# Kernel optimization log

Measured on AMD Instinct MI355X. Metric: run time of the kernel, lower is better.

Reference implementation:

```python
import jax, jax.numpy as jnp
import numpy as np
from jax import lax

N_NOTES, N_WORDS, BATCH = 64, 256, 32
WORDS_DIM, VOCAB = 128, 50000
OC, FW = 256, 3          # conv output channels, filter width
H, NCLS = 256, 2         # GRU hidden, target classes


def setup_inputs() -> dict:
    key = jax.random.key(0)
    ks = jax.random.split(key, 18)
    s = 0.05
    nrm = lambda k, shp: (jax.random.normal(k, shp, dtype=jnp.float32) * s)
    return {
        "mini_batch": jax.random.randint(ks[0], (N_NOTES, N_WORDS, BATCH), 0, VOCAB),
        "hidden_state": jnp.zeros((2, BATCH, H), jnp.float32),
        "embed_table": nrm(ks[1], (VOCAB, WORDS_DIM)),
        "conv_w": nrm(ks[2], (OC, 1, FW, WORDS_DIM)),
        "conv_b": nrm(ks[3], (OC,)),
        "w_ih_f": nrm(ks[4], (3 * H, OC)), "w_hh_f": nrm(ks[5], (3 * H, H)),
        "b_ih_f": nrm(ks[6], (3 * H,)),   "b_hh_f": nrm(ks[7], (3 * H,)),
        "w_ih_b": nrm(ks[8], (3 * H, OC)), "w_hh_b": nrm(ks[9], (3 * H, H)),
        "b_ih_b": nrm(ks[10], (3 * H,)),  "b_hh_b": nrm(ks[11], (3 * H,)),
        "W_note": nrm(ks[12], (2 * H, 2 * H)),
        "bias_note": nrm(ks[13], (2 * H,)),
        "proj_note": nrm(ks[14], (2 * H,)),
        "lin_w": nrm(ks[15], (NCLS, 2 * H)),
        "lin_b": nrm(ks[16], (NCLS,)),
    }


def _gru_scan(xs, h0, w_ih, w_hh, b_ih, b_hh, reverse=False):
    # xs: [N, B, in], h0: [B, H]; standard PyTorch GRU cell math.
    def step(h, x):
        gi = x @ w_ih.T + b_ih
        gh = h @ w_hh.T + b_hh
        ir, iz, i_n = jnp.split(gi, 3, axis=-1)
        hr, hz, h_n = jnp.split(gh, 3, axis=-1)
        r = jax.nn.sigmoid(ir + hr)
        z = jax.nn.sigmoid(iz + hz)
        n = jnp.tanh(i_n + r * h_n)
        h_new = (1.0 - z) * n + z * h
        return h_new, h_new
    _, ys = lax.scan(step, h0, xs, reverse=reverse)
    return ys  # [N, B, H]


def reference(mini_batch, hidden_state, embed_table, conv_w, conv_b,
              w_ih_f, w_hh_f, b_ih_f, b_hh_f,
              w_ih_b, w_hh_b, b_ih_b, b_hh_b,
              W_note, bias_note, proj_note, lin_w, lin_b):
    N, Wd, B = mini_batch.shape
    toks = mini_batch.transpose(0, 2, 1)                 # [N, B, Wd]
    emb = embed_table[toks]                              # [N, B, Wd, D] -- big gather
    x = emb.reshape(N * B, 1, Wd, WORDS_DIM)             # NCHW
    y = lax.conv_general_dilated(
        x, conv_w, window_strides=(1, 1),
        padding=((FW - 1, FW - 1), (0, 0)),
        dimension_numbers=("NCHW", "OIHW", "NCHW"))     # [N*B, OC, L, 1]
    y = jnp.tanh(y + conv_b[None, :, None, None])[..., 0]  # [N*B, OC, L]
    feat = y.max(axis=2).reshape(N, B, -1)               # max-pool over words -> [N, B, OC]

    out_f = _gru_scan(feat, hidden_state[0], w_ih_f, w_hh_f, b_ih_f, b_hh_f)
    out_b = _gru_scan(feat, hidden_state[1], w_ih_b, w_hh_b, b_ih_b, b_hh_b, reverse=True)
    out_note = jnp.concatenate([out_f, out_b], axis=-1)  # [N, B, 2H]

    # additive attention over notes (fused version of the per-step python loops)
    squish = jnp.tanh(jnp.einsum("nbd,de->nbe", out_note, W_note) + bias_note)
    attn = jnp.einsum("nbe,e->nb", squish, proj_note)    # [N, B]
    note_attn_norm = jax.nn.softmax(attn.T, axis=1)      # [B, N], softmax over notes
    note_attn_vectors = jnp.einsum("nb,nbd->bd", note_attn_norm.T, out_note)  # [B, 2H]
    final_map = note_attn_vectors @ lin_w.T + lin_b      # [B, NCLS]
    return (out_note, note_attn_norm, note_attn_vectors, final_map)
```

## Files before the change

kernel.cpp:

```cpp
#include <hip/hip_runtime.h>

#define NN 64
#define NW 256
#define NB 32
#define WD 128
#define OCH 256
#define HD 256
#define G3 768

typedef __attribute__((ext_vector_type(8))) __bf16 bf16x8;
typedef __attribute__((ext_vector_type(4))) __bf16 bf16x4;
typedef __attribute__((ext_vector_type(4))) float  f32x4;

__device__ __forceinline__ float sigm(float x){ return 1.f/(1.f + __expf(-x)); }
__device__ __forceinline__ float tanh_(float x){
  float xx = fminf(fmaxf(x, -15.f), 15.f);
  float e = __expf(-2.f*xx);
  return (1.f - e)/(1.f + e);
}
__device__ __forceinline__ bf16x8 pack8(f32x4 a, f32x4 b){
  bf16x8 v;
  v[0]=(__bf16)a[0]; v[1]=(__bf16)a[1]; v[2]=(__bf16)a[2]; v[3]=(__bf16)a[3];
  v[4]=(__bf16)b[0]; v[5]=(__bf16)b[1]; v[6]=(__bf16)b[2]; v[7]=(__bf16)b[3];
  return v;
}
__device__ __forceinline__ void gload_lds16(const void* g, void* l){
  __builtin_amdgcn_global_load_lds(
      (const __attribute__((address_space(1))) unsigned int*)g,
      (__attribute__((address_space(3))) unsigned int*)l, 16, 0, 0);
}

#define EMB_ELEMS 6400000
#define CW_ELEMS  98304
__global__ void k0_cvt(const float* __restrict__ emb, const float* __restrict__ cw,
                       __bf16* __restrict__ embb, __bf16* __restrict__ cwb)
{
  long e8 = ((long)blockIdx.x*256 + threadIdx.x)*8;
  if (e8 < EMB_ELEMS) {
    f32x4 a = *(const f32x4*)(emb + e8); f32x4 b = *(const f32x4*)(emb + e8 + 4);
    *(bf16x8*)(embb + e8) = pack8(a, b);
  } else if (e8 < EMB_ELEMS + CW_ELEMS) {
    long o = e8 - EMB_ELEMS;
    f32x4 a = *(const f32x4*)(cw + o); f32x4 b = *(const f32x4*)(cw + o + 4);
    *(bf16x8*)(cwb + o) = pack8(a, b);
  }
}

__global__ __launch_bounds__(512, 2) void k1_conv(
    const int* __restrict__ mb, const __bf16* __restrict__ embb,
    const __bf16* __restrict__ cwb, const float* __restrict__ cb,
    __bf16* __restrict__ feat)
{
  __shared__ int tok[NW];
  __shared__ __bf16 A[274*128];
  const int blk = blockIdx.x, n = blk >> 5, b = blk & 31;
  const int t = threadIdx.x, wv = t >> 6, l = t & 63;
  const int lo = l & 15, hi = l >> 4;
  if (t < NW) tok[t] = mb[(n*NW + t)*NB + b];
  if (t < 288) {
    int rr = t >> 4, c = t & 15;
    int row = (rr < 2) ? rr : (256 + rr);
    f32x4 z = {0.f,0.f,0.f,0.f};
    *(f32x4*)((char*)A + row*256 + c*16) = z;
  }
  __syncthreads();
  #pragma unroll
  for (int rr = 0; rr < 8; ++rr) {
    const int w = wv*32 + rr*4 + hi;
    const int row = w + 2;
    const __bf16* src = embb + (long)tok[w]*WD + ((lo ^ (row & 7)) << 3);
    gload_lds16(src, &A[(wv*32 + rr*4 + 2)*128]);
  }
  __syncthreads();
  const int ocb = wv*32;
  bf16x8 B[2][12];
  #pragma unroll
  for (int nt = 0; nt < 2; ++nt) {
    int oc = ocb + nt*16 + lo;
    #pragma unroll
    for (int kf = 0; kf < 12; ++kf)
      B[nt][kf] = *(const bf16x8*)(cwb + oc*384 + kf*32 + hi*8);
  }
  f32x4 mx0 = {-3e38f,-3e38f,-3e38f,-3e38f}, mx1 = mx0;
  for (int mt = 0; mt < 17; ++mt) {
    bf16x8 Af[12];
    const int lrow = mt*16 + lo;
    #pragma unroll
    for (int kf = 0; kf < 12; ++kf) {
      int prow = lrow + (kf >> 2);
      int ch = (kf & 3)*4 + hi;
      Af[kf] = *(const bf16x8*)((char*)A + prow*256 + ((ch ^ (prow & 7)) << 4));
    }
    f32x4 a0 = {0,0,0,0}, a1 = {0,0,0,0};
    #pragma unroll
    for (int kf = 0; kf < 12; ++kf) {
      a0 = __builtin_amdgcn_mfma_f32_16x16x32_bf16(Af[kf], B[0][kf], a0, 0,0,0);
      a1 = __builtin_amdgcn_mfma_f32_16x16x32_bf16(Af[kf], B[1][kf], a1, 0,0,0);
    }
    const int rbase = mt*16 + hi*4;
    #pragma unroll
    for (int r = 0; r < 4; ++r) {
      if (rbase + r < 258) {
        mx0[r] = fmaxf(mx0[r], a0[r]);
        mx1[r] = fmaxf(mx1[r], a1[r]);
      }
    }
  }
  float v0 = fmaxf(fmaxf(mx0[0], mx0[1]), fmaxf(mx0[2], mx0[3]));
  float v1 = fmaxf(fmaxf(mx1[0], mx1[1]), fmaxf(mx1[2], mx1[3]));
  v0 = fmaxf(v0, __shfl_xor(v0, 16)); v0 = fmaxf(v0, __shfl_xor(v0, 32));
  v1 = fmaxf(v1, __shfl_xor(v1, 16)); v1 = fmaxf(v1, __shfl_xor(v1, 32));
  if (l < 16) {
    const int m = n*NB + b;
    feat[m*OCH + ocb + l]      = (__bf16)tanh_(v0 + cb[ocb + l]);
    feat[m*OCH + ocb + 16 + l] = (__bf16)tanh_(v1 + cb[ocb + 16 + l]);
  }
}

__global__ __launch_bounds__(256, 2) void k2_gi(
    const __bf16* __restrict__ feat,
    const float* __restrict__ wihf, const float* __restrict__ bihf, const float* __restrict__ bhhf,
    const float* __restrict__ wihb, const float* __restrict__ bihb, const float* __restrict__ bhhb,
    float* __restrict__ gi_t)
{
  const int bid = blockIdx.x;
  const int mblk = bid & 31, cblk = bid >> 5;
  const int dir = (cblk >= 12) ? 1 : 0;
  const int jb = (cblk - dir*12)*64;
  const float* wih = dir ? wihb : wihf;
  const float* bih = dir ? bihb : bihf;
  const float* bhh = dir ? bhhb : bhhf;
  const int t = threadIdx.x, wv = t >> 6, l = t & 63;
  const int lo = l & 15, hi = l >> 4;
  const int mbase = mblk*64 + wv*16;
  bf16x8 Af[8];
  #pragma unroll
  for (int kf = 0; kf < 8; ++kf)
    Af[kf] = *(const bf16x8*)(feat + (mbase + lo)*HD + kf*32 + hi*8);
  bf16x8 Bf[4][8];
  #pragma unroll
  for (int nt = 0; nt < 4; ++nt) {
    int j = jb + nt*16 + lo;
    #pragma unroll
    for (int kf = 0; kf < 8; ++kf) {
      const float* src = wih + j*HD + kf*32 + hi*8;
      Bf[nt][kf] = pack8(*(const f32x4*)src, *(const f32x4*)(src + 4));
    }
  }
  f32x4 acc[4];
  #pragma unroll
  for (int nt = 0; nt < 4; ++nt) { f32x4 z = {0,0,0,0}; acc[nt] = z; }
  #pragma unroll
  for (int kf = 0; kf < 8; ++kf)
    #pragma unroll
    for (int nt = 0; nt < 4; ++nt)
      acc[nt] = __builtin_amdgcn_mfma_f32_16x16x32_bf16(Af[kf], Bf[nt][kf], acc[nt], 0,0,0);
  #pragma unroll
  for (int nt = 0; nt < 4; ++nt) {
    int j = jb + nt*16 + lo;
    float bias = bih[j] + (j < 512 ? bhh[j] : 0.f);
    #pragma unroll
    for (int r = 0; r < 4; ++r) {
      int m = mbase + hi*4 + r;
      int note = m >> 5, bb = m & 31;
      gi_t[(((long)dir*NN + note)*G3 + j)*NB + bb] = acc[nt][r] + bias;
    }
  }
}

__global__ __launch_bounds__(512, 1) void k3_gru(
    const float* __restrict__ gi_t,
    const float* __restrict__ whhf, const float* __restrict__ bhhf,
    const float* __restrict__ whhb, const float* __restrict__ bhhb,
    const float* __restrict__ hid,
    float* __restrict__ out, __bf16* __restrict__ onbf)
{
  const int blk = blockIdx.x;
  const int dir = blk >> 1, mtb = blk & 1;
  const float* whh = dir ? whhb : whhf;
  const float* bhh = dir ? bhhb : bhhf;
  const int t = threadIdx.x, wv = t >> 6, l = t & 63;
  const int lo = l & 15, hi = l >> 4;
  __shared__ __bf16 hb[2][16*256];

  bf16x8 Bf[3][2][8];
  #pragma unroll
  for (int g = 0; g < 3; ++g)
    #pragma unroll
    for (int q = 0; q < 2; ++q) {
      const int col = g*256 + wv*32 + q*16 + lo;
      #pragma unroll
      for (int kf = 0; kf < 8; ++kf) {
        const float* src = whh + col*HD + kf*32 + hi*8;
        Bf[g][q][kf] = pack8(*(const f32x4*)src, *(const f32x4*)(src + 4));
      }
    }
  const float bnh0 = bhh[512 + wv*32 + lo];
  const float bnh1 = bhh[512 + wv*32 + 16 + lo];

  f32x4 h[2];
  #pragma unroll
  for (int q = 0; q < 2; ++q)
    #pragma unroll
    for (int r = 0; r < 4; ++r)
      h[q][r] = hid[dir*(NB*HD) + (mtb*16 + hi*4 + r)*HD + wv*32 + q*16 + lo];

  #pragma unroll
  for (int q = 0; q < 2; ++q) {
    const int j = wv*32 + q*16 + lo;
    #pragma unroll
    for (int r = 0; r < 4; ++r) {
      const int row = hi*4 + r;
      *(__bf16*)((char*)&hb[0][0] + row*512 + (((j >> 3) ^ (row & 7)) << 4) + (j & 7)*2)
          = (__bf16)h[q][r];
    }
  }

  const float* gbase = gi_t + (long)dir*NN*G3*NB + mtb*16 + hi*4;
  f32x4 P[3][2];
  {
    const int note0 = dir ? 63 : 0;
    #pragma unroll
    for (int g = 0; g < 3; ++g)
      #pragma unroll
      for (int q = 0; q < 2; ++q)
        P[g][q] = *(const f32x4*)(gbase + ((long)note0*G3 + g*256 + wv*32 + q*16 + lo)*NB);
  }
  __syncthreads();

  int cur = 0;
  for (int st = 0; st < 64; ++st) {
    const int note = dir ? 63 - st : st;
    f32x4 acc[3][2];
    #pragma unroll
    for (int g = 0; g < 3; ++g)
      #pragma unroll
      for (int q = 0; q < 2; ++q) { f32x4 z = {0,0,0,0}; acc[g][q] = z; }
    const char* hbc = (const char*)&hb[cur][0];
    #pragma unroll
    for (int kf = 0; kf < 8; ++kf) {
      const int ch = kf*4 + hi;
      bf16x8 Afr = *(const bf16x8*)(hbc + lo*512 + ((ch ^ (lo & 7)) << 4));
      #pragma unroll
      for (int g = 0; g < 3; ++g)
        #pragma unroll
        for (int q = 0; q < 2; ++q)
          acc[g][q] = __builtin_amdgcn_mfma_f32_16x16x32_bf16(Afr, Bf[g][q][kf], acc[g][q], 0,0,0);
    }
    char* hbn = (char*)&hb[cur ^ 1][0];
    #pragma unroll
    for (int q = 0; q < 2; ++q) {
      const int j = wv*32 + q*16 + lo;
      const float bn = q ? bnh1 : bnh0;
      #pragma unroll
      for (int r = 0; r < 4; ++r) {
        float rr = sigm(P[0][q][r] + acc[0][q][r]);
        float zz = sigm(P[1][q][r] + acc[1][q][r]);
        float nn = tanh_(P[2][q][r] + rr*(acc[2][q][r] + bn));
        float hv = (1.f - zz)*nn + zz*h[q][r];
        h[q][r] = hv;
        const int row = hi*4 + r;
        __bf16 hbf = (__bf16)hv;
        *(__bf16*)(hbn + row*512 + (((j >> 3) ^ (row & 7)) << 4) + (j & 7)*2) = hbf;
        const long oidx = (long)(note*NB + mtb*16 + row)*512 + dir*HD + j;
        out[oidx] = hv;
        onbf[oidx] = hbf;
      }
    }
    const int nst = (st < 63) ? st + 1 : 63;
    const int nnote = dir ? 63 - nst : nst;
    #pragma unroll
    for (int g = 0; g < 3; ++g)
      #pragma unroll
      for (int q = 0; q < 2; ++q)
        P[g][q] = *(const f32x4*)(gbase + ((long)nnote*G3 + g*256 + wv*32 + q*16 + lo)*NB);
    __syncthreads();
    cur ^= 1;
  }
}

__global__ void k4pre(const float* __restrict__ Wn, __bf16* __restrict__ Wt){
  int idx = blockIdx.x*256 + threadIdx.x;
  int e = idx >> 9, d = idx & 511;
  Wt[e*512 + d] = (__bf16)Wn[d*512 + e];
}

__global__ __launch_bounds__(256, 2) void k4a(
    const __bf16* __restrict__ onbf, const __bf16* __restrict__ Wt,
    const float* __restrict__ bn, const float* __restrict__ pj,
    float* __restrict__ attn)
{
  const int mbase = blockIdx.x*16;
  const int t = threadIdx.x, wv = t >> 6, l = t & 63;
  bf16x8 Af[16];
  #pragma unroll
  for (int kf = 0; kf < 16; ++kf)
    Af[kf] = *(const bf16x8*)(onbf + (mbase + (l & 15))*512 + kf*32 + (l >> 4)*8);
  float aa0=0, aa1=0, aa2=0, aa3=0;
  #pragma unroll 1
  for (int ntl = 0; ntl < 8; ++ntl) {
    const int e = wv*128 + ntl*16 + (l & 15);
    const float be = bn[e], pe = pj[e];
    f32x4 acc = {0,0,0,0};
    #pragma unroll
    for (int kf = 0; kf < 16; ++kf) {
      bf16x8 Bfr = *(const bf16x8*)(Wt + e*512 + kf*32 + (l >> 4)*8);
      acc = __builtin_amdgcn_mfma_f32_16x16x32_bf16(Af[kf], Bfr, acc, 0,0,0);
    }
    aa0 += tanh_(acc[0] + be)*pe;
    aa1 += tanh_(acc[1] + be)*pe;
    aa2 += tanh_(acc[2] + be)*pe;
    aa3 += tanh_(acc[3] + be)*pe;
  }
  #pragma unroll
  for (int msk = 8; msk >= 1; msk >>= 1) {
    aa0 += __shfl_xor(aa0, msk); aa1 += __shfl_xor(aa1, msk);
    aa2 += __shfl_xor(aa2, msk); aa3 += __shfl_xor(aa3, msk);
  }
  __shared__ float part[4][16];
  if ((l & 15) == 0) {
    int rb = (l >> 4)*4;
    part[wv][rb+0]=aa0; part[wv][rb+1]=aa1; part[wv][rb+2]=aa2; part[wv][rb+3]=aa3;
  }
  __syncthreads();
  if (t < 16) attn[mbase + t] = part[0][t] + part[1][t] + part[2][t] + part[3][t];
}

__global__ __launch_bounds__(512) void k4b(
    const float* __restrict__ attn, const float* __restrict__ lw, const float* __restrict__ lb,
    float* __restrict__ out)
{
  const int b = blockIdx.x, t = threadIdx.x;
  __shared__ float wl[64];
  __shared__ float vl[512];
  if (t < 64) {
    float a = attn[t*NB + b];
    float mx = a;
    #pragma unroll
    for (int msk = 32; msk >= 1; msk >>= 1) mx = fmaxf(mx, __shfl_xor(mx, msk));
    float ex = __expf(a - mx);
    float s = ex;
    #pragma unroll
    for (int msk = 32; msk >= 1; msk >>= 1) s += __shfl_xor(s, msk);
    float w = ex / s;
    out[1048576 + b*64 + t] = w;
    wl[t] = w;
  }
  __syncthreads();
  {
    float acc = 0.f;
    #pragma unroll 1
    for (int n = 0; n < 64; ++n) acc += wl[n]*out[(n*NB + b)*512 + t];
    out[1050624 + b*512 + t] = acc;
    vl[t] = acc;
  }
  __syncthreads();
  if (t < 128) {
    int c = t >> 6, ln = t & 63;
    float p = 0.f;
    for (int d = ln; d < 512; d += 64) p += vl[d]*lw[c*512 + d];
    #pragma unroll
    for (int msk = 32; msk >= 1; msk >>= 1) p += __shfl_xor(p, msk);
    if (ln == 0) out[1067008 + b*2 + c] = p + lb[c];
  }
}

extern "C" void kernel_launch(void* const* d_in, const int* in_sizes, int n_in,
                              void* d_out, int out_size, void* d_ws, size_t ws_size,
                              hipStream_t stream) {
  const int*   mb   = (const int*)d_in[0];
  const float* hid  = (const float*)d_in[1];
  const float* emb  = (const float*)d_in[2];
  const float* cw   = (const float*)d_in[3];
  const float* cb   = (const float*)d_in[4];
  const float* wihf = (const float*)d_in[5];
  const float* whhf = (const float*)d_in[6];
  const float* bihf = (const float*)d_in[7];
  const float* bhhf = (const float*)d_in[8];
  const float* wihb = (const float*)d_in[9];
  const float* whhb = (const float*)d_in[10];
  const float* bihb = (const float*)d_in[11];
  const float* bhhb = (const float*)d_in[12];
  const float* Wn   = (const float*)d_in[13];
  const float* bnote= (const float*)d_in[14];
  const float* pj   = (const float*)d_in[15];
  const float* lw   = (const float*)d_in[16];
  const float* lb   = (const float*)d_in[17];
  float* out = (float*)d_out;
  char* ws = (char*)d_ws;
  __bf16* feat = (__bf16*)ws;
  __bf16* embb = (__bf16*)(ws + 1048576);
  float*  gi_t = (float*)(ws + 1048576);
  __bf16* onbf = (__bf16*)(ws + 13848576);
  float*  attn = (float*)(ws + 15945728);
  __bf16* Wt   = (__bf16*)(ws + 15953920);
  __bf16* cwb  = (__bf16*)(ws + 16478208);

  k0_cvt<<<3173, 256, 0, stream>>>(emb, cw, embb, cwb);
  k1_conv<<<2048, 512, 0, stream>>>(mb, embb, cwb, cb, feat);
  k2_gi<<<768, 256, 0, stream>>>(feat, wihf, bihf, bhhf, wihb, bihb, bhhb, gi_t);
  k4pre<<<1024, 256, 0, stream>>>(Wn, Wt);
  k3_gru<<<4, 512, 0, stream>>>(gi_t, whhf, bhhf, whhb, bhhb, hid, out, onbf);
  k4a<<<128, 256, 0, stream>>>(onbf, Wt, bnote, pj, attn);
  k4b<<<32, 512, 0, stream>>>(attn, lw, lb, out);
}
```

Baseline: 696.2 us.

## Prefetch GRU input gates into LDS asynchronously and drop bf16 output copy

The gate-input buffer is re-laid out in 16-row batch tiles so each GRU block can copy the next timestep's tile straight into double-buffered LDS with async global-to-LDS loads. The per-step barrier then waits only for the older loads, instead of pulling register prefetches through the serial loop. The separate bf16 copy of the GRU output is removed, and the attention kernel now reads the fp32 output and converts it itself. The launch bound changes to 2 blocks per CU, which limits registers and could spill the large resident recurrent-weight fragments.

```diff
diff --git a/kernel.cpp b/kernel.cpp
--- a/kernel.cpp
+++ b/kernel.cpp
@@ -163,17 +163,17 @@
     for (int r = 0; r < 4; ++r) {
       int m = mbase + hi*4 + r;
       int note = m >> 5, bb = m & 31;
-      gi_t[(((long)dir*NN + note)*G3 + j)*NB + bb] = acc[nt][r] + bias;
-    }
-  }
-}
-
-__global__ __launch_bounds__(512, 1) void k3_gru(
+      gi_t[((((long)dir*NN + note)*2 + (bb >> 4))*G3 + j)*16 + (bb & 15)] = acc[nt][r] + bias;
+    }
+  }
+}
+
+__global__ __launch_bounds__(512, 2) void k3_gru(
     const float* __restrict__ gi_t,
     const float* __restrict__ whhf, const float* __restrict__ bhhf,
     const float* __restrict__ whhb, const float* __restrict__ bhhb,
     const float* __restrict__ hid,
-    float* __restrict__ out, __bf16* __restrict__ onbf)
+    float* __restrict__ out)
 {
   const int blk = blockIdx.x;
   const int dir = blk >> 1, mtb = blk & 1;
@@ -182,6 +182,7 @@
   const int t = threadIdx.x, wv = t >> 6, l = t & 63;
   const int lo = l & 15, hi = l >> 4;
   __shared__ __bf16 hb[2][16*256];
+  __shared__ float  gib[2][G3*16];
 
   bf16x8 Bf[3][2][8];
   #pragma unroll
@@ -216,21 +217,26 @@
     }
   }
 
-  const float* gbase = gi_t + (long)dir*NN*G3*NB + mtb*16 + hi*4;
-  f32x4 P[3][2];
-  {
-    const int note0 = dir ? 63 : 0;
-    #pragma unroll
-    for (int g = 0; g < 3; ++g)
-      #pragma unroll
-      for (int q = 0; q < 2; ++q)
-        P[g][q] = *(const f32x4*)(gbase + ((long)note0*G3 + g*256 + wv*32 + q*16 + lo)*NB);
+  const long gtile = ((long)(dir*NN + (dir ? 63 : 0))*2 + mtb)*(G3*16);
+  #pragma unroll
+  for (int p = 0; p < 6; ++p) {
+    const int c = (p*8 + wv)*256;
+    gload_lds16(gi_t + gtile + c + l*4, &gib[0][c]);
   }
   __syncthreads();
 
   int cur = 0;
   for (int st = 0; st < 64; ++st) {
     const int note = dir ? 63 - st : st;
+    if (st < 63) {
+      const int nnote = dir ? 62 - st : st + 1;
+      const long gt2 = ((long)(dir*NN + nnote)*2 + mtb)*(G3*16);
+      #pragma unroll
+      for (int p = 0; p < 6; ++p) {
+        const int c = (p*8 + wv)*256;
+        gload_lds16(gi_t + gt2 + c + l*4, &gib[cur ^ 1][c]);
+      }
+    }
     f32x4 acc[3][2];
     #pragma unroll
     for (int g = 0; g < 3; ++g)
@@ -248,33 +254,27 @@
           acc[g][q] = __builtin_amdgcn_mfma_f32_16x16x32_bf16(Afr, Bf[g][q][kf], acc[g][q], 0,0,0);
     }
     char* hbn = (char*)&hb[cur ^ 1][0];
+    const float* gcur = &gib[cur][0];
     #pragma unroll
     for (int q = 0; q < 2; ++q) {
-      const int j = wv*32 + q*16 + lo;
+      const int jH = wv*32 + q*16 + lo;
+      f32x4 ir  = *(const f32x4*)(gcur + (jH        )*16 + hi*4);
+      f32x4 iz  = *(const f32x4*)(gcur + (jH + 256  )*16 + hi*4);
+      f32x4 in_ = *(const f32x4*)(gcur + (jH + 512  )*16 + hi*4);
       const float bn = q ? bnh1 : bnh0;
       #pragma unroll
       for (int r = 0; r < 4; ++r) {
-        float rr = sigm(P[0][q][r] + acc[0][q][r]);
-        float zz = sigm(P[1][q][r] + acc[1][q][r]);
-        float nn = tanh_(P[2][q][r] + rr*(acc[2][q][r] + bn));
+        float rr = sigm(ir[r] + acc[0][q][r]);
+        float zz = sigm(iz[r] + acc[1][q][r]);
+        float nn = tanh_(in_[r] + rr*(acc[2][q][r] + bn));
         float hv = (1.f - zz)*nn + zz*h[q][r];
         h[q][r] = hv;
         const int row = hi*4 + r;
-        __bf16 hbf = (__bf16)hv;
-        *(__bf16*)(hbn + row*512 + (((j >> 3) ^ (row & 7)) << 4) + (j & 7)*2) = hbf;
-        const long oidx = (long)(note*NB + mtb*16 + row)*512 + dir*HD + j;
-        out[oidx] = hv;
-        onbf[oidx] = hbf;
+        *(__bf16*)(hbn + row*512 + (((jH >> 3) ^ (row & 7)) << 4) + (jH & 7)*2) = (__bf16)hv;
+        out[(long)(note*NB + mtb*16 + row)*512 + dir*HD + jH] = hv;
       }
     }
-    const int nst = (st < 63) ? st + 1 : 63;
-    const int nnote = dir ? 63 - nst : nst;
-    #pragma unroll
-    for (int g = 0; g < 3; ++g)
-      #pragma unroll
-      for (int q = 0; q < 2; ++q)
-        P[g][q] = *(const f32x4*)(gbase + ((long)nnote*G3 + g*256 + wv*32 + q*16 + lo)*NB);
-    __syncthreads();
+    asm volatile("s_waitcnt vmcnt(8) lgkmcnt(0)\n\ts_barrier" ::: "memory");
     cur ^= 1;
   }
 }
@@ -286,7 +286,7 @@
 }
 
 __global__ __launch_bounds__(256, 2) void k4a(
-    const __bf16* __restrict__ onbf, const __bf16* __restrict__ Wt,
+    const float* __restrict__ onf, const __bf16* __restrict__ Wt,
     const float* __restrict__ bn, const float* __restrict__ pj,
     float* __restrict__ attn)
 {
@@ -294,8 +294,10 @@
   const int t = threadIdx.x, wv = t >> 6, l = t & 63;
   bf16x8 Af[16];
   #pragma unroll
-  for (int kf = 0; kf < 16; ++kf)
-    Af[kf] = *(const bf16x8*)(onbf + (mbase + (l & 15))*512 + kf*32 + (l >> 4)*8);
+  for (int kf = 0; kf < 16; ++kf) {
+    const float* src = onf + (mbase + (l & 15))*512 + kf*32 + (l >> 4)*8;
+    Af[kf] = pack8(*(const f32x4*)src, *(const f32x4*)(src + 4));
+  }
   float aa0=0, aa1=0, aa2=0, aa3=0;
   #pragma unroll 1
   for (int ntl = 0; ntl < 8; ++ntl) {
@@ -391,16 +393,15 @@
   __bf16* feat = (__bf16*)ws;
   __bf16* embb = (__bf16*)(ws + 1048576);
   float*  gi_t = (float*)(ws + 1048576);
-  __bf16* onbf = (__bf16*)(ws + 13848576);
-  float*  attn = (float*)(ws + 15945728);
-  __bf16* Wt   = (__bf16*)(ws + 15953920);
-  __bf16* cwb  = (__bf16*)(ws + 16478208);
+  float*  attn = (float*)(ws + 13848576);
+  __bf16* Wt   = (__bf16*)(ws + 13856768);
+  __bf16* cwb  = (__bf16*)(ws + 14380800);
 
   k0_cvt<<<3173, 256, 0, stream>>>(emb, cw, embb, cwb);
   k1_conv<<<2048, 512, 0, stream>>>(mb, embb, cwb, cb, feat);
   k2_gi<<<768, 256, 0, stream>>>(feat, wihf, bihf, bhhf, wihb, bihb, bhhb, gi_t);
   k4pre<<<1024, 256, 0, stream>>>(Wn, Wt);
-  k3_gru<<<4, 512, 0, stream>>>(gi_t, whhf, bhhf, whhb, bhhb, hid, out, onbf);
-  k4a<<<128, 256, 0, stream>>>(onbf, Wt, bnote, pj, attn);
+  k3_gru<<<4, 512, 0, stream>>>(gi_t, whhf, bhhf, whhb, bhhb, hid, out);
+  k4a<<<128, 256, 0, stream>>>(out, Wt, bnote, pj, attn);
   k4b<<<32, 512, 0, stream>>>(attn, lw, lb, out);
 }
```

New measurement: 615.8 us. 11.5% less time.
